# Kernel optimization log

Hardware: AMD Instinct MI355X
Metric: run time of the kernel (lower is better)

The kernel has to match this reference:

```python
import jax, jax.numpy as jnp
import numpy as np

N = 50000   # nodes
E = 600000  # edges
F = 128     # feat_in
H = 64      # hidden_features
H2 = 32     # hidden_features // 2


def setup_inputs() -> dict:
    key = jax.random.key(0)
    ks = jax.random.split(key, 10)
    w = lambda k, shape: jax.random.normal(k, shape, dtype=jnp.float32) * 0.05
    return {
        "x": jax.random.normal(ks[0], (N, F), dtype=jnp.float32),
        "edge_index": jax.random.randint(ks[1], (2, E), 0, N, dtype=jnp.int32),
        "edge_attr": jax.random.uniform(ks[2], (E, 1), dtype=jnp.float32),
        # GINConv 1 MLP: Linear(F,H) -> Linear(H,H), learnable eps
        "w1a": w(ks[3], (H, F)), "b1a": jnp.zeros((H,), jnp.float32),
        "w1b": w(ks[4], (H, H)), "b1b": jnp.zeros((H,), jnp.float32),
        "eps1": jnp.zeros((), jnp.float32),
        # GINConv 2 MLP: Linear(H,H2) -> Linear(H2,H2), learnable eps
        "w2a": w(ks[5], (H2, H)), "b2a": jnp.zeros((H2,), jnp.float32),
        "w2b": w(ks[6], (H2, H2)), "b2b": jnp.zeros((H2,), jnp.float32),
        "eps2": jnp.zeros((), jnp.float32),
        # SAGEConv(H2, 1): lin_l (neighbor path, has bias), lin_r (root path, no bias)
        "wl": w(ks[7], (1, H2)), "bl": jnp.zeros((1,), jnp.float32),
        "wr": w(ks[8], (1, H2)),
    }


def _gin(x, src, dst, eps, wa, ba, wb, bb):
    # GIN: MLP((1+eps)*x_i + sum_{j->i} x_j)
    agg = jax.ops.segment_sum(x[src], dst, num_segments=x.shape[0])
    h = (1.0 + eps) * x + agg
    h = h @ wa.T + ba
    return h @ wb.T + bb


def reference(x, edge_index, edge_attr, w1a, b1a, w1b, b1b, eps1,
              w2a, b2a, w2b, b2b, eps2, wl, bl, wr):
    src, dst = edge_index[0], edge_index[1]
    ew = edge_attr.squeeze()  # (E,)
    n = x.shape[0]

    h = jax.nn.relu(_gin(x, src, dst, eps1, w1a, b1a, w1b, b1b))
    # dropout is identity in eval mode
    h = jax.nn.relu(_gin(h, src, dst, eps2, w2a, b2a, w2b, b2b))

    # SAGEConv with edge weights: mean over weighted messages + root transform
    msg = ew[:, None] * h[src]                                   # (E, H2)
    num = jax.ops.segment_sum(msg, dst, num_segments=n)          # (N, H2)
    cnt = jax.ops.segment_sum(jnp.ones((msg.shape[0],), h.dtype), dst, num_segments=n)
    mean = num / jnp.maximum(cnt, 1.0)[:, None]
    out = mean @ wl.T + bl + h @ wr.T                            # (N, 1)
    return jax.nn.relu(out)
```

## Files before the change

### kernel.cpp

```cpp
#include <hip/hip_runtime.h>

#define N_NODES 50000
#define N_EDGES 600000
#define F_IN 128
#define H1 64
#define H2 32
#define NBLK ((N_NODES + 255) / 256)
#define PREP_BLOCKS 41
#define CNT_BLOCKS ((N_EDGES / 4 + 255) / 256)
#define GEMM1_BLOCKS ((N_NODES + 63) / 64)
#define FILL_BLOCKS ((N_EDGES / 4 + 255) / 256)

__device__ inline unsigned bf_round(float x) {
  unsigned u = __float_as_uint(x);
  u += 0x7FFFu + ((u >> 16) & 1u);
  return u >> 16;
}
__device__ inline unsigned pack_bf2(float a, float b) {
  return (bf_round(b) << 16) | bf_round(a);
}
__device__ inline float2 unpack_bf2(unsigned u) {
  return make_float2(__uint_as_float(u << 16), __uint_as_float(u & 0xFFFF0000u));
}

__global__ __launch_bounds__(256) void prep_and_count(
    const float* __restrict__ w1a, const float* __restrict__ b1a,
    const float* __restrict__ w1b, const float* __restrict__ b1b,
    const float* __restrict__ w2a, const float* __restrict__ b2a,
    const float* __restrict__ w2b, const float* __restrict__ b2b,
    float* __restrict__ M1, float* __restrict__ c1,
    float* __restrict__ M2, float* __restrict__ c2,
    const int* __restrict__ ei, int* __restrict__ counts) {
  if (blockIdx.x >= PREP_BLOCKS) {
    int t = (blockIdx.x - PREP_BLOCKS) * 256 + threadIdx.x;
    if (t < N_EDGES / 4) {
      int4 d4 = *reinterpret_cast<const int4*>(&ei[N_EDGES + t * 4]);
      atomicAdd(&counts[d4.x], 1);
      atomicAdd(&counts[d4.y], 1);
      atomicAdd(&counts[d4.z], 1);
      atomicAdd(&counts[d4.w], 1);
    }
    return;
  }
  int i = blockIdx.x * 256 + threadIdx.x;
  if (i < F_IN * H1) {
    int f = i >> 6, h = i & 63;
    float s = 0.f;
    for (int m = 0; m < H1; ++m) s += w1a[m * F_IN + f] * w1b[h * H1 + m];
    M1[i] = s;
    return;
  }
  i -= F_IN * H1;
  if (i < H1) {
    float s = b1b[i];
    for (int m = 0; m < H1; ++m) s += b1a[m] * w1b[i * H1 + m];
    c1[i] = s;
    return;
  }
  i -= H1;
  if (i < H1 * H2) {
    int h = i >> 5, o = i & 31;
    float s = 0.f;
    for (int m = 0; m < H2; ++m) s += w2a[m * H1 + h] * w2b[o * H2 + m];
    M2[i] = s;
    return;
  }
  i -= H1 * H2;
  if (i < H2) {
    float s = b2b[i];
    for (int m = 0; m < H2; ++m) s += b2a[m] * w2b[i * H2 + m];
    c2[i] = s;
  }
}

__global__ __launch_bounds__(256) void block_sums(const int* __restrict__ counts,
                                                  int* __restrict__ bsums) {
  __shared__ int s[256];
  int t = threadIdx.x;
  int i = blockIdx.x * 256 + t;
  s[t] = (i < N_NODES) ? counts[i] : 0;
  __syncthreads();
  for (int off = 128; off > 0; off >>= 1) {
    if (t < off) s[t] += s[t + off];
    __syncthreads();
  }
  if (t == 0) bsums[blockIdx.x] = s[0];
}

__global__ __launch_bounds__(256) void scan_bsums(const int* __restrict__ bsums,
                                                  int* __restrict__ boffs,
                                                  int* __restrict__ row_ptr) {
  __shared__ int s[256];
  int t = threadIdx.x;
  int v = (t < NBLK) ? bsums[t] : 0;
  s[t] = v;
  __syncthreads();
  for (int off = 1; off < 256; off <<= 1) {
    int u = (t >= off) ? s[t - off] : 0;
    __syncthreads();
    s[t] += u;
    __syncthreads();
  }
  if (t < NBLK) boffs[t] = s[t] - v;
  if (t == 255) row_ptr[N_NODES] = s[255];
}

__global__ __launch_bounds__(256) void emit_rowptr(const int* __restrict__ counts,
                                                   const int* __restrict__ boffs,
                                                   int* __restrict__ row_ptr,
                                                   int* __restrict__ cursor) {
  __shared__ int s[256];
  int t = threadIdx.x;
  int i = blockIdx.x * 256 + t;
  int v = (i < N_NODES) ? counts[i] : 0;
  s[t] = v;
  __syncthreads();
  for (int off = 1; off < 256; off <<= 1) {
    int u = (t >= off) ? s[t - off] : 0;
    __syncthreads();
    s[t] += u;
    __syncthreads();
  }
  if (i < N_NODES) {
    int ex = boffs[blockIdx.x] + s[t] - v;
    row_ptr[i] = ex;
    cursor[i] = ex;
  }
}

__global__ __launch_bounds__(256) void gemm1_fill(
    const float* __restrict__ x, const float* __restrict__ M1,
    unsigned* __restrict__ ybf, const int* __restrict__ ei,
    const float* __restrict__ ea, int* __restrict__ cursor,
    int2* __restrict__ csr) {
  __shared__ float sW[F_IN * H1];
  __shared__ float sX[32][H1];
  if (blockIdx.x >= GEMM1_BLOCKS) {
    int t = (blockIdx.x - GEMM1_BLOCKS) * 256 + threadIdx.x;
    if (t < N_EDGES / 4) {
      int4 s4 = *reinterpret_cast<const int4*>(&ei[4 * t]);
      int4 d4 = *reinterpret_cast<const int4*>(&ei[N_EDGES + 4 * t]);
      float4 w4 = *reinterpret_cast<const float4*>(&ea[4 * t]);
      int p0 = atomicAdd(&cursor[d4.x], 1);
      csr[p0] = make_int2(s4.x, __float_as_int(w4.x));
      int p1 = atomicAdd(&cursor[d4.y], 1);
      csr[p1] = make_int2(s4.y, __float_as_int(w4.y));
      int p2 = atomicAdd(&cursor[d4.z], 1);
      csr[p2] = make_int2(s4.z, __float_as_int(w4.z));
      int p3 = atomicAdd(&cursor[d4.w], 1);
      csr[p3] = make_int2(s4.w, __float_as_int(w4.w));
    }
    return;
  }
  int tid = threadIdx.x;
  for (int i = tid; i < F_IN * H1; i += 256) sW[i] = M1[i];

  int row0 = blockIdx.x * 64;
  int tr = tid >> 4;
  int tc = tid & 15;
  int lrow = tid & 63;
  int kgrp = tid >> 6;
  const float* xrow = x + (long long)(row0 + lrow) * F_IN;
  bool rvalid = (row0 + lrow) < N_NODES;

  float acc[4][4] = {{0.f}};

  for (int kc = 0; kc < 4; ++kc) {
    float4 v0 = make_float4(0.f, 0.f, 0.f, 0.f);
    float4 v1 = make_float4(0.f, 0.f, 0.f, 0.f);
    if (rvalid) {
      v0 = *reinterpret_cast<const float4*>(xrow + kc * 32 + kgrp * 8);
      v1 = *reinterpret_cast<const float4*>(xrow + kc * 32 + kgrp * 8 + 4);
    }
    __syncthreads();
    sX[kgrp * 8 + 0][lrow] = v0.x;
    sX[kgrp * 8 + 1][lrow] = v0.y;
    sX[kgrp * 8 + 2][lrow] = v0.z;
    sX[kgrp * 8 + 3][lrow] = v0.w;
    sX[kgrp * 8 + 4][lrow] = v1.x;
    sX[kgrp * 8 + 5][lrow] = v1.y;
    sX[kgrp * 8 + 6][lrow] = v1.z;
    sX[kgrp * 8 + 7][lrow] = v1.w;
    __syncthreads();
#pragma unroll
    for (int k = 0; k < 32; ++k) {
      float4 a = *reinterpret_cast<const float4*>(&sX[k][tr * 4]);
      float4 b = *reinterpret_cast<const float4*>(&sW[(kc * 32 + k) * H1 + tc * 4]);
      acc[0][0] += a.x * b.x; acc[0][1] += a.x * b.y;
      acc[0][2] += a.x * b.z; acc[0][3] += a.x * b.w;
      acc[1][0] += a.y * b.x; acc[1][1] += a.y * b.y;
      acc[1][2] += a.y * b.z; acc[1][3] += a.y * b.w;
      acc[2][0] += a.z * b.x; acc[2][1] += a.z * b.y;
      acc[2][2] += a.z * b.z; acc[2][3] += a.z * b.w;
      acc[3][0] += a.w * b.x; acc[3][1] += a.w * b.y;
      acc[3][2] += a.w * b.z; acc[3][3] += a.w * b.w;
    }
  }
#pragma unroll
  for (int i = 0; i < 4; ++i) {
    int row = row0 + tr * 4 + i;
    if (row < N_NODES) {
      uint2 o;
      o.x = pack_bf2(acc[i][0], acc[i][1]);
      o.y = pack_bf2(acc[i][2], acc[i][3]);
      *reinterpret_cast<uint2*>(&ybf[(unsigned)row * 32 + tc * 2]) = o;
    }
  }
}

__global__ __launch_bounds__(256) void agg_h(
    const unsigned* __restrict__ ybf, const int* __restrict__ row_ptr,
    const int2* __restrict__ csr, const float* __restrict__ c1,
    const float* __restrict__ eps1p, float* __restrict__ h) {
  int tid = threadIdx.x;
  int node = blockIdx.x * 4 + (tid >> 6);
  if (node >= N_NODES) return;
  int lane = tid & 63;
  int half = lane >> 5;
  int j = lane & 31;
  int start = row_ptr[node], end = row_ptr[node + 1];
  int mid = start + ((end - start + 1) >> 1);
  int b0 = half ? mid : start;
  int b1 = half ? end : mid;
  float a0 = 0.f, a1 = 0.f;
  int e = b0;
  for (; e + 4 <= b1; e += 4) {
    int s0 = csr[e + 0].x;
    int s1 = csr[e + 1].x;
    int s2 = csr[e + 2].x;
    int s3 = csr[e + 3].x;
    float2 u0 = unpack_bf2(ybf[(unsigned)s0 * 32 + j]);
    float2 u1 = unpack_bf2(ybf[(unsigned)s1 * 32 + j]);
    float2 u2 = unpack_bf2(ybf[(unsigned)s2 * 32 + j]);
    float2 u3 = unpack_bf2(ybf[(unsigned)s3 * 32 + j]);
    a0 += (u0.x + u1.x) + (u2.x + u3.x);
    a1 += (u0.y + u1.y) + (u2.y + u3.y);
  }
  float2 t0 = make_float2(0.f, 0.f), t1 = make_float2(0.f, 0.f),
         t2 = make_float2(0.f, 0.f);
  if (e + 0 < b1) t0 = unpack_bf2(ybf[(unsigned)csr[e + 0].x * 32 + j]);
  if (e + 1 < b1) t1 = unpack_bf2(ybf[(unsigned)csr[e + 1].x * 32 + j]);
  if (e + 2 < b1) t2 = unpack_bf2(ybf[(unsigned)csr[e + 2].x * 32 + j]);
  a0 += (t0.x + t1.x) + t2.x;
  a1 += (t0.y + t1.y) + t2.y;
  a0 += __shfl_xor(a0, 32);
  a1 += __shfl_xor(a1, 32);
  if (half == 0) {
    float eps1 = 1.0f + *eps1p;
    float2 self = unpack_bf2(ybf[(unsigned)node * 32 + j]);
    float2 c = *reinterpret_cast<const float2*>(&c1[2 * j]);
    float2 hv;
    hv.x = fmaxf(eps1 * self.x + a0 + c.x, 0.f);
    hv.y = fmaxf(eps1 * self.y + a1 + c.y, 0.f);
    *reinterpret_cast<float2*>(&h[(unsigned)node * H1 + 2 * j]) = hv;
  }
}

__global__ __launch_bounds__(256) void gemm2(const float* __restrict__ h,
                                             const float* __restrict__ M2,
                                             unsigned* __restrict__ zbf) {
  __shared__ float sW[H1 * H2];
  __shared__ float sX[H1][64];
  int tid = threadIdx.x;
  for (int i = tid; i < H1 * H2; i += 256) sW[i] = M2[i];

  int row0 = blockIdx.x * 64;
  int lrow = tid & 63;
  int kg = tid >> 6;
  bool rv = (row0 + lrow) < N_NODES;
  float4 v[4] = {};
  if (rv) {
    const float* hr = h + (long long)(row0 + lrow) * H1 + kg * 16;
#pragma unroll
    for (int q = 0; q < 4; ++q) v[q] = *reinterpret_cast<const float4*>(hr + q * 4);
  }
#pragma unroll
  for (int q = 0; q < 4; ++q) {
    sX[kg * 16 + q * 4 + 0][lrow] = v[q].x;
    sX[kg * 16 + q * 4 + 1][lrow] = v[q].y;
    sX[kg * 16 + q * 4 + 2][lrow] = v[q].z;
    sX[kg * 16 + q * 4 + 3][lrow] = v[q].w;
  }
  __syncthreads();
  int tr = tid >> 4;
  int tc = tid & 15;
  float acc[4][2] = {{0.f}};
#pragma unroll
  for (int k = 0; k < H1; ++k) {
    float4 a = *reinterpret_cast<const float4*>(&sX[k][tr * 4]);
    float2 b = *reinterpret_cast<const float2*>(&sW[k * H2 + tc * 2]);
    acc[0][0] += a.x * b.x; acc[0][1] += a.x * b.y;
    acc[1][0] += a.y * b.x; acc[1][1] += a.y * b.y;
    acc[2][0] += a.z * b.x; acc[2][1] += a.z * b.y;
    acc[3][0] += a.w * b.x; acc[3][1] += a.w * b.y;
  }
#pragma unroll
  for (int i = 0; i < 4; ++i) {
    int row = row0 + tr * 4 + i;
    if (row < N_NODES)
      zbf[(unsigned)row * 16 + tc] = pack_bf2(acc[i][0], acc[i][1]);
  }
}

__global__ __launch_bounds__(256) void gin3(
    const unsigned* __restrict__ zbf, const int* __restrict__ row_ptr,
    const int2* __restrict__ csr, const float* __restrict__ c2,
    const float* __restrict__ eps2p, const float* __restrict__ wl,
    const float* __restrict__ wr, float* __restrict__ p,
    float* __restrict__ r) {
  int tid = blockIdx.x * 256 + threadIdx.x;
  int node = tid >> 4;
  if (node >= N_NODES) return;
  int j = tid & 15;
  int start = row_ptr[node], end = row_ptr[node + 1];
  float a0 = 0.f, a1 = 0.f;
  int e = start;
  for (; e + 8 <= end; e += 8) {
    int s0 = csr[e + 0].x; int s1 = csr[e + 1].x;
    int s2 = csr[e + 2].x; int s3 = csr[e + 3].x;
    int s4 = csr[e + 4].x; int s5 = csr[e + 5].x;
    int s6 = csr[e + 6].x; int s7 = csr[e + 7].x;
    float2 u0 = unpack_bf2(zbf[(unsigned)s0 * 16 + j]);
    float2 u1 = unpack_bf2(zbf[(unsigned)s1 * 16 + j]);
    float2 u2 = unpack_bf2(zbf[(unsigned)s2 * 16 + j]);
    float2 u3 = unpack_bf2(zbf[(unsigned)s3 * 16 + j]);
    float2 u4 = unpack_bf2(zbf[(unsigned)s4 * 16 + j]);
    float2 u5 = unpack_bf2(zbf[(unsigned)s5 * 16 + j]);
    float2 u6 = unpack_bf2(zbf[(unsigned)s6 * 16 + j]);
    float2 u7 = unpack_bf2(zbf[(unsigned)s7 * 16 + j]);
    a0 += ((u0.x + u1.x) + (u2.x + u3.x)) + ((u4.x + u5.x) + (u6.x + u7.x));
    a1 += ((u0.y + u1.y) + (u2.y + u3.y)) + ((u4.y + u5.y) + (u6.y + u7.y));
  }
  for (; e + 4 <= end; e += 4) {
    int s0 = csr[e + 0].x; int s1 = csr[e + 1].x;
    int s2 = csr[e + 2].x; int s3 = csr[e + 3].x;
    float2 u0 = unpack_bf2(zbf[(unsigned)s0 * 16 + j]);
    float2 u1 = unpack_bf2(zbf[(unsigned)s1 * 16 + j]);
    float2 u2 = unpack_bf2(zbf[(unsigned)s2 * 16 + j]);
    float2 u3 = unpack_bf2(zbf[(unsigned)s3 * 16 + j]);
    a0 += (u0.x + u1.x) + (u2.x + u3.x);
    a1 += (u0.y + u1.y) + (u2.y + u3.y);
  }
  float2 t0 = make_float2(0.f, 0.f), t1 = make_float2(0.f, 0.f),
         t2 = make_float2(0.f, 0.f);
  if (e + 0 < end) t0 = unpack_bf2(zbf[(unsigned)csr[e + 0].x * 16 + j]);
  if (e + 1 < end) t1 = unpack_bf2(zbf[(unsigned)csr[e + 1].x * 16 + j]);
  if (e + 2 < end) t2 = unpack_bf2(zbf[(unsigned)csr[e + 2].x * 16 + j]);
  a0 += (t0.x + t1.x) + t2.x;
  a1 += (t0.y + t1.y) + t2.y;
  float eps2 = 1.0f + *eps2p;
  float2 self = unpack_bf2(zbf[(unsigned)node * 16 + j]);
  float2 c = *reinterpret_cast<const float2*>(&c2[2 * j]);
  float h0 = fmaxf(eps2 * self.x + a0 + c.x, 0.f);
  float h1 = fmaxf(eps2 * self.y + a1 + c.y, 0.f);
  float2 l = *reinterpret_cast<const float2*>(&wl[2 * j]);
  float2 w = *reinterpret_cast<const float2*>(&wr[2 * j]);
  float pd = h0 * l.x + h1 * l.y;
  float rd = h0 * w.x + h1 * w.y;
#pragma unroll
  for (int m = 8; m >= 1; m >>= 1) {
    pd += __shfl_xor(pd, m, 16);
    rd += __shfl_xor(rd, m, 16);
  }
  if (j == 0) {
    p[node] = pd;
    r[node] = rd;
  }
}

__global__ __launch_bounds__(256) void sage_out(
    const int* __restrict__ row_ptr, const int2* __restrict__ csr,
    const float* __restrict__ p, const float* __restrict__ r,
    const float* __restrict__ blp, float* __restrict__ out) {
  int idx = blockIdx.x * 256 + threadIdx.x;
  int node = idx >> 4;
  if (node >= N_NODES) return;
  int l = idx & 15;
  int start = row_ptr[node], end = row_ptr[node + 1];
  float acc = 0.f;
  for (int e = start + l; e < end; e += 16) {
    int2 c = csr[e];
    acc += __int_as_float(c.y) * p[c.x];
  }
#pragma unroll
  for (int m = 8; m >= 1; m >>= 1) acc += __shfl_xor(acc, m, 16);
  if (l == 0) {
    float mean = acc / fmaxf((float)(end - start), 1.0f);
    out[node] = fmaxf(mean + blp[0] + r[node], 0.f);
  }
}

extern "C" void kernel_launch(void* const* d_in, const int* in_sizes, int n_in,
                              void* d_out, int out_size, void* d_ws,
                              size_t ws_size, hipStream_t stream) {
  const float* x = (const float*)d_in[0];
  const int* ei = (const int*)d_in[1];
  const float* ea = (const float*)d_in[2];
  const float* w1a = (const float*)d_in[3];
  const float* b1a = (const float*)d_in[4];
  const float* w1b = (const float*)d_in[5];
  const float* b1b = (const float*)d_in[6];
  const float* eps1 = (const float*)d_in[7];
  const float* w2a = (const float*)d_in[8];
  const float* b2a = (const float*)d_in[9];
  const float* w2b = (const float*)d_in[10];
  const float* b2b = (const float*)d_in[11];
  const float* eps2 = (const float*)d_in[12];
  const float* wl = (const float*)d_in[13];
  const float* bl = (const float*)d_in[14];
  const float* wr = (const float*)d_in[15];
  float* out = (float*)d_out;

  float* ws = (float*)d_ws;
  float* M1 = ws;
  float* c1 = M1 + F_IN * H1;
  float* M2 = c1 + H1;
  float* c2 = M2 + H1 * H2;
  unsigned* ybf = (unsigned*)(c2 + H2);
  float* h = (float*)(ybf + (size_t)N_NODES * 32);
  unsigned* zbf = (unsigned*)(h + (size_t)N_NODES * H1);
  float* p = (float*)(zbf + (size_t)N_NODES * 16);
  float* r = p + N_NODES;
  int2* csr = (int2*)(r + N_NODES);
  int* counts = (int*)(csr + N_EDGES);
  int* cursor = counts + N_NODES;
  int* bsums = cursor + N_NODES;
  int* boffs = bsums + NBLK;
  int* row_ptr = boffs + NBLK;

  hipMemsetAsync(counts, 0, sizeof(int) * (size_t)N_NODES, stream);

  prep_and_count<<<PREP_BLOCKS + CNT_BLOCKS, 256, 0, stream>>>(
      w1a, b1a, w1b, b1b, w2a, b2a, w2b, b2b, M1, c1, M2, c2, ei, counts);

  block_sums<<<NBLK, 256, 0, stream>>>(counts, bsums);
  scan_bsums<<<1, 256, 0, stream>>>(bsums, boffs, row_ptr);
  emit_rowptr<<<NBLK, 256, 0, stream>>>(counts, boffs, row_ptr, cursor);

  gemm1_fill<<<GEMM1_BLOCKS + FILL_BLOCKS, 256, 0, stream>>>(
      x, M1, ybf, ei, ea, cursor, csr);

  agg_h<<<(N_NODES + 3) / 4, 256, 0, stream>>>(ybf, row_ptr, csr, c1, eps1, h);

  gemm2<<<(N_NODES + 63) / 64, 256, 0, stream>>>(h, M2, zbf);

  gin3<<<(N_NODES * 16 + 255) / 256, 256, 0, stream>>>(zbf, row_ptr, csr, c2,
                                                       eps2, wl, wr, p, r);

  sage_out<<<(N_NODES * 16 + 255) / 256, 256, 0, stream>>>(row_ptr, csr, p, r,
                                                           bl, out);
}
```

Measured before the change: 223.9 us.

## Fuse GIN1 aggregation with GEMM2 and fold block-offset scan into rowptr emit

```diff
diff --git a/kernel.cpp b/kernel.cpp
--- a/kernel.cpp
+++ b/kernel.cpp
@@ -87,30 +87,24 @@
   if (t == 0) bsums[blockIdx.x] = s[0];
 }
 
-__global__ __launch_bounds__(256) void scan_bsums(const int* __restrict__ bsums,
-                                                  int* __restrict__ boffs,
-                                                  int* __restrict__ row_ptr) {
+__global__ __launch_bounds__(256) void emit_rowptr(const int* __restrict__ counts,
+                                                   const int* __restrict__ bsums,
+                                                   int* __restrict__ row_ptr,
+                                                   int* __restrict__ cursor) {
+  __shared__ int sb[256];
   __shared__ int s[256];
   int t = threadIdx.x;
-  int v = (t < NBLK) ? bsums[t] : 0;
-  s[t] = v;
+  int bv = (t < NBLK) ? bsums[t] : 0;
+  sb[t] = bv;
   __syncthreads();
   for (int off = 1; off < 256; off <<= 1) {
-    int u = (t >= off) ? s[t - off] : 0;
-    __syncthreads();
-    s[t] += u;
-    __syncthreads();
-  }
-  if (t < NBLK) boffs[t] = s[t] - v;
-  if (t == 255) row_ptr[N_NODES] = s[255];
-}
-
-__global__ __launch_bounds__(256) void emit_rowptr(const int* __restrict__ counts,
-                                                   const int* __restrict__ boffs,
-                                                   int* __restrict__ row_ptr,
-                                                   int* __restrict__ cursor) {
-  __shared__ int s[256];
-  int t = threadIdx.x;
+    int u = (t >= off) ? sb[t - off] : 0;
+    __syncthreads();
+    sb[t] += u;
+    __syncthreads();
+  }
+  if (blockIdx.x == 0 && t == NBLK - 1) row_ptr[N_NODES] = sb[t];
+  int boff = (blockIdx.x == 0) ? 0 : sb[blockIdx.x - 1];
   int i = blockIdx.x * 256 + t;
   int v = (i < N_NODES) ? counts[i] : 0;
   s[t] = v;
@@ -122,7 +116,7 @@
     __syncthreads();
   }
   if (i < N_NODES) {
-    int ex = boffs[blockIdx.x] + s[t] - v;
+    int ex = boff + s[t] - v;
     row_ptr[i] = ex;
     cursor[i] = ex;
   }
@@ -208,86 +202,75 @@
   }
 }
 
-__global__ __launch_bounds__(256) void agg_h(
+__global__ __launch_bounds__(256) void gin2(
     const unsigned* __restrict__ ybf, const int* __restrict__ row_ptr,
-    const int2* __restrict__ csr, const float* __restrict__ c1,
-    const float* __restrict__ eps1p, float* __restrict__ h) {
+    const int2* __restrict__ csr, const float* __restrict__ M2,
+    const float* __restrict__ c1, const float* __restrict__ eps1p,
+    unsigned* __restrict__ zbf) {
+  __shared__ float sW[H1 * H2];
+  __shared__ float sh[H1][68];
   int tid = threadIdx.x;
-  int node = blockIdx.x * 4 + (tid >> 6);
-  if (node >= N_NODES) return;
+  for (int i = tid; i < H1 * H2; i += 256) sW[i] = M2[i];
+
+  int row0 = blockIdx.x * 64;
+  int wave = tid >> 6;
   int lane = tid & 63;
   int half = lane >> 5;
   int j = lane & 31;
-  int start = row_ptr[node], end = row_ptr[node + 1];
-  int mid = start + ((end - start + 1) >> 1);
-  int b0 = half ? mid : start;
-  int b1 = half ? end : mid;
-  float a0 = 0.f, a1 = 0.f;
-  int e = b0;
-  for (; e + 4 <= b1; e += 4) {
-    int s0 = csr[e + 0].x;
-    int s1 = csr[e + 1].x;
-    int s2 = csr[e + 2].x;
-    int s3 = csr[e + 3].x;
-    float2 u0 = unpack_bf2(ybf[(unsigned)s0 * 32 + j]);
-    float2 u1 = unpack_bf2(ybf[(unsigned)s1 * 32 + j]);
-    float2 u2 = unpack_bf2(ybf[(unsigned)s2 * 32 + j]);
-    float2 u3 = unpack_bf2(ybf[(unsigned)s3 * 32 + j]);
-    a0 += (u0.x + u1.x) + (u2.x + u3.x);
-    a1 += (u0.y + u1.y) + (u2.y + u3.y);
-  }
-  float2 t0 = make_float2(0.f, 0.f), t1 = make_float2(0.f, 0.f),
-         t2 = make_float2(0.f, 0.f);
-  if (e + 0 < b1) t0 = unpack_bf2(ybf[(unsigned)csr[e + 0].x * 32 + j]);
-  if (e + 1 < b1) t1 = unpack_bf2(ybf[(unsigned)csr[e + 1].x * 32 + j]);
-  if (e + 2 < b1) t2 = unpack_bf2(ybf[(unsigned)csr[e + 2].x * 32 + j]);
-  a0 += (t0.x + t1.x) + t2.x;
-  a1 += (t0.y + t1.y) + t2.y;
-  a0 += __shfl_xor(a0, 32);
-  a1 += __shfl_xor(a1, 32);
-  if (half == 0) {
-    float eps1 = 1.0f + *eps1p;
-    float2 self = unpack_bf2(ybf[(unsigned)node * 32 + j]);
-    float2 c = *reinterpret_cast<const float2*>(&c1[2 * j]);
-    float2 hv;
-    hv.x = fmaxf(eps1 * self.x + a0 + c.x, 0.f);
-    hv.y = fmaxf(eps1 * self.y + a1 + c.y, 0.f);
-    *reinterpret_cast<float2*>(&h[(unsigned)node * H1 + 2 * j]) = hv;
-  }
-}
-
-__global__ __launch_bounds__(256) void gemm2(const float* __restrict__ h,
-                                             const float* __restrict__ M2,
-                                             unsigned* __restrict__ zbf) {
-  __shared__ float sW[H1 * H2];
-  __shared__ float sX[H1][64];
-  int tid = threadIdx.x;
-  for (int i = tid; i < H1 * H2; i += 256) sW[i] = M2[i];
-
-  int row0 = blockIdx.x * 64;
-  int lrow = tid & 63;
-  int kg = tid >> 6;
-  bool rv = (row0 + lrow) < N_NODES;
-  float4 v[4] = {};
-  if (rv) {
-    const float* hr = h + (long long)(row0 + lrow) * H1 + kg * 16;
-#pragma unroll
-    for (int q = 0; q < 4; ++q) v[q] = *reinterpret_cast<const float4*>(hr + q * 4);
-  }
-#pragma unroll
-  for (int q = 0; q < 4; ++q) {
-    sX[kg * 16 + q * 4 + 0][lrow] = v[q].x;
-    sX[kg * 16 + q * 4 + 1][lrow] = v[q].y;
-    sX[kg * 16 + q * 4 + 2][lrow] = v[q].z;
-    sX[kg * 16 + q * 4 + 3][lrow] = v[q].w;
+  float eps1 = 1.0f + *eps1p;
+  float2 c = *reinterpret_cast<const float2*>(&c1[2 * j]);
+
+  for (int rnd = 0; rnd < 16; ++rnd) {
+    int nl = rnd * 4 + wave;
+    int node = row0 + nl;
+    float a0 = 0.f, a1 = 0.f;
+    if (node < N_NODES) {
+      int start = row_ptr[node], end = row_ptr[node + 1];
+      int mid = start + ((end - start + 1) >> 1);
+      int b0 = half ? mid : start;
+      int b1 = half ? end : mid;
+      int e = b0;
+      for (; e + 4 <= b1; e += 4) {
+        int s0 = csr[e + 0].x;
+        int s1 = csr[e + 1].x;
+        int s2 = csr[e + 2].x;
+        int s3 = csr[e + 3].x;
+        float2 u0 = unpack_bf2(ybf[(unsigned)s0 * 32 + j]);
+        float2 u1 = unpack_bf2(ybf[(unsigned)s1 * 32 + j]);
+        float2 u2 = unpack_bf2(ybf[(unsigned)s2 * 32 + j]);
+        float2 u3 = unpack_bf2(ybf[(unsigned)s3 * 32 + j]);
+        a0 += (u0.x + u1.x) + (u2.x + u3.x);
+        a1 += (u0.y + u1.y) + (u2.y + u3.y);
+      }
+      float2 t0 = make_float2(0.f, 0.f), t1 = make_float2(0.f, 0.f),
+             t2 = make_float2(0.f, 0.f);
+      if (e + 0 < b1) t0 = unpack_bf2(ybf[(unsigned)csr[e + 0].x * 32 + j]);
+      if (e + 1 < b1) t1 = unpack_bf2(ybf[(unsigned)csr[e + 1].x * 32 + j]);
+      if (e + 2 < b1) t2 = unpack_bf2(ybf[(unsigned)csr[e + 2].x * 32 + j]);
+      a0 += (t0.x + t1.x) + t2.x;
+      a1 += (t0.y + t1.y) + t2.y;
+    }
+    a0 += __shfl_xor(a0, 32);
+    a1 += __shfl_xor(a1, 32);
+    if (half == 0) {
+      float h0 = 0.f, h1 = 0.f;
+      if (node < N_NODES) {
+        float2 self = unpack_bf2(ybf[(unsigned)node * 32 + j]);
+        h0 = fmaxf(eps1 * self.x + a0 + c.x, 0.f);
+        h1 = fmaxf(eps1 * self.y + a1 + c.y, 0.f);
+      }
+      sh[2 * j][nl] = h0;
+      sh[2 * j + 1][nl] = h1;
+    }
   }
   __syncthreads();
+
   int tr = tid >> 4;
   int tc = tid & 15;
   float acc[4][2] = {{0.f}};
 #pragma unroll
   for (int k = 0; k < H1; ++k) {
-    float4 a = *reinterpret_cast<const float4*>(&sX[k][tr * 4]);
+    float4 a = *reinterpret_cast<const float4*>(&sh[k][tr * 4]);
     float2 b = *reinterpret_cast<const float2*>(&sW[k * H2 + tc * 2]);
     acc[0][0] += a.x * b.x; acc[0][1] += a.x * b.y;
     acc[1][0] += a.y * b.x; acc[1][1] += a.y * b.y;
@@ -417,16 +400,14 @@
   float* M2 = c1 + H1;
   float* c2 = M2 + H1 * H2;
   unsigned* ybf = (unsigned*)(c2 + H2);
-  float* h = (float*)(ybf + (size_t)N_NODES * 32);
-  unsigned* zbf = (unsigned*)(h + (size_t)N_NODES * H1);
+  unsigned* zbf = ybf + (size_t)N_NODES * 32;
   float* p = (float*)(zbf + (size_t)N_NODES * 16);
   float* r = p + N_NODES;
   int2* csr = (int2*)(r + N_NODES);
   int* counts = (int*)(csr + N_EDGES);
   int* cursor = counts + N_NODES;
   int* bsums = cursor + N_NODES;
-  int* boffs = bsums + NBLK;
-  int* row_ptr = boffs + NBLK;
+  int* row_ptr = bsums + NBLK;
 
   hipMemsetAsync(counts, 0, sizeof(int) * (size_t)N_NODES, stream);
 
@@ -434,15 +415,13 @@
       w1a, b1a, w1b, b1b, w2a, b2a, w2b, b2b, M1, c1, M2, c2, ei, counts);
 
   block_sums<<<NBLK, 256, 0, stream>>>(counts, bsums);
-  scan_bsums<<<1, 256, 0, stream>>>(bsums, boffs, row_ptr);
-  emit_rowptr<<<NBLK, 256, 0, stream>>>(counts, boffs, row_ptr, cursor);
+  emit_rowptr<<<NBLK, 256, 0, stream>>>(counts, bsums, row_ptr, cursor);
 
   gemm1_fill<<<GEMM1_BLOCKS + FILL_BLOCKS, 256, 0, stream>>>(
       x, M1, ybf, ei, ea, cursor, csr);
 
-  agg_h<<<(N_NODES + 3) / 4, 256, 0, stream>>>(ybf, row_ptr, csr, c1, eps1, h);
-
-  gemm2<<<(N_NODES + 63) / 64, 256, 0, stream>>>(h, M2, zbf);
+  gin2<<<(N_NODES + 63) / 64, 256, 0, stream>>>(ybf, row_ptr, csr, M2, c1,
+                                                eps1, zbf);
 
   gin3<<<(N_NODES * 16 + 255) / 256, 256, 0, stream>>>(zbf, row_ptr, csr, c2,
                                                        eps2, wl, wr, p, r);
```

Result: slower. 324.4 us (+44.9%).
